# Kernel tuning notes

Measured on AMD Instinct MI355X. Metric: run time of the kernel, lower is better.

Reference implementation:

```python
import jax, jax.numpy as jnp
import numpy as np
from jax import lax

SD = 16  # sample_duration
POOL_KS = (SD, SD * 3 // 4, SD // 2, SD // 4)  # (16, 12, 8, 4)


def conv3d_same(x, w, b):
    # x: [B,C,T,H,W], w: [O,I,3,3,3]
    y = lax.conv_general_dilated(
        x, w, window_strides=(1, 1, 1), padding=[(1, 1), (1, 1), (1, 1)],
        dimension_numbers=("NCDHW", "OIDHW", "NCDHW"))
    return y + b[None, :, None, None, None]


def maxpool_t(x, k):
    # MaxPool3d((k,1,1), stride=1): max over sliding temporal window
    return lax.reduce_window(x, -jnp.inf, lax.max,
                             (1, 1, k, 1, 1), (1, 1, 1, 1, 1), "VALID")


def head1x1(x, w, b):
    # 1x1x1 Conv3d as einsum; x: [B,C,T,H,W], w: [O,C]
    return jnp.einsum("bcthw,oc->bothw", x, w) + b[None, :, None, None, None]


def cls_prob(score):
    # _RPN.reshape(x,2) -> softmax(dim=1) -> reshape back to [B,30,T,H,W]
    B, C, T, H, W = score.shape
    s2 = score.reshape(B, 2, (C * T) // 2, H, W)
    p = jax.nn.softmax(s2, axis=1)
    return p.reshape(B, C, T, H, W)


def setup_inputs() -> dict:
    key = jax.random.key(0)
    ks = jax.random.split(key, 12)
    din, B, H, W = 512, 2, 28, 28
    s = 0.05
    return {
        "base_feat": jax.random.normal(ks[0], (B, din, SD, H, W), jnp.float32),
        "im_info": jnp.ones((B, 3), jnp.float32) * 448.0,
        "gt_boxes": jax.random.uniform(ks[1], (B, 20, 5), jnp.float32),
        "gt_rois": jax.random.uniform(ks[2], (B, 20, SD, 5), jnp.float32),
        "W_conv": jax.random.normal(ks[3], (din, din, 3, 3, 3), jnp.float32) * 0.01,
        "b_conv": jnp.zeros((din,), jnp.float32),
        "W_cls": jax.random.normal(ks[4], (30, din), jnp.float32) * s,
        "b_cls": jnp.zeros((30,), jnp.float32),
        "W_bbox": jax.random.normal(ks[5], (960, din), jnp.float32) * s,
        "b_bbox": jnp.zeros((960,), jnp.float32),
        "W_bbox_34": jax.random.normal(ks[6], (720, din), jnp.float32) * s,
        "b_bbox_34": jnp.zeros((720,), jnp.float32),
        "W_bbox_2": jax.random.normal(ks[7], (480, din), jnp.float32) * s,
        "b_bbox_2": jnp.zeros((480,), jnp.float32),
        "W_bbox_4": jax.random.normal(ks[8], (240, din), jnp.float32) * s,
        "b_bbox_4": jnp.zeros((240,), jnp.float32),
    }


def reference(base_feat, im_info, gt_boxes, gt_rois,
              W_conv, b_conv, W_cls, b_cls,
              W_bbox, b_bbox, W_bbox_34, b_bbox_34,
              W_bbox_2, b_bbox_2, W_bbox_4, b_bbox_4):
    # RPN conv + relu
    x = jax.nn.relu(conv3d_same(base_feat, W_conv, b_conv))
    # four temporal max-pool branches (T' = 1, 5, 9, 13)
    pools = [maxpool_t(x, k) for k in POOL_KS]
    # NOTE: original code applies the SAME RPN_cls_score conv to all branches
    probs = tuple(cls_prob(head1x1(p, W_cls, b_cls)) for p in pools)
    bbox_ws = [(W_bbox, b_bbox), (W_bbox_34, b_bbox_34),
               (W_bbox_2, b_bbox_2), (W_bbox_4, b_bbox_4)]
    bboxes = tuple(head1x1(p, w, b) for p, (w, b) in zip(pools, bbox_ws))
    return probs + bboxes
```

## Files before the change

### kernel.cpp

```cpp
#include <hip/hip_runtime.h>

typedef unsigned short u16;
typedef unsigned int   u32;
typedef __bf16  bf16x8 __attribute__((ext_vector_type(8)));
typedef float   f32x4  __attribute__((ext_vector_type(4)));

__device__ __forceinline__ float bf2f(u16 u) {
    u32 v = ((u32)u) << 16;
    return __builtin_bit_cast(float, v);
}
__device__ __forceinline__ u16 f2bf(float f) {
    u32 u = __builtin_bit_cast(u32, f);
    return (u16)((u + 0x7FFFu + ((u >> 16) & 1u)) >> 16);
}
__device__ __forceinline__ float ldf(const void* p, long i, int f32) {
    return f32 ? ((const float*)p)[i] : bf2f(((const u16*)p)[i]);
}
__device__ __forceinline__ int is_f32(const u32* im) {
    return im[0] == 0x43E00000u;
}
__device__ __forceinline__ void gl2lds16(const u16* g, u16* l) {
    __builtin_amdgcn_global_load_lds(
        (const __attribute__((address_space(1))) void*)g,
        (__attribute__((address_space(3))) void*)l, 16, 0, 0);
}

__global__ void zero_kernel(uint4* __restrict__ p, const int n)
{
    int i = blockIdx.x * 256 + threadIdx.x;
    if (i < n) p[i] = uint4{0u, 0u, 0u, 0u};
}

__global__ void pad_fill(const void* __restrict__ src, u16* __restrict__ xpad,
                         const u32* __restrict__ im)
{
    const int f32 = is_f32(im);
    __shared__ u16 lds[56 * 40];
    int blk = blockIdx.x;
    const int h2  = blk % 14;  blk /= 14;
    const int c32 = blk & 15;  blk >>= 4;
    const int t   = blk & 15;
    const int b   = blk >> 4;
    const int tid = threadIdx.x;
    const long sbase = ((long)(b * 512 + c32 * 32) * 16 + t) * 784 + h2 * 56;
    #pragma unroll
    for (int it = tid; it < 1792; it += 256) {
        const int c = it / 56, p = it - c * 56;
        float v = f32 ? ((const float*)src)[sbase + (long)c * 12544 + p]
                      : bf2f(((const u16*)src)[sbase + (long)c * 12544 + p]);
        lds[p * 40 + c] = f2bf(v);
    }
    __syncthreads();
    if (tid < 224) {
        const int p = tid >> 2, g = tid & 3;
        const int h = h2 * 2 + p / 28, w = p % 28;
        const long o = (((long)(b * 18 + t + 1) * 30 + h + 1) * 30 + (w + 1)) * 512
                       + c32 * 32 + g * 8;
        *(uint4*)&xpad[o] = *(const uint4*)&lds[p * 40 + g * 8];
    }
}

__global__ void wt_transform(const void* __restrict__ wconv, u16* __restrict__ wt,
                             const u32* __restrict__ im)
{
    const int f32 = is_f32(im);
    __shared__ u16 lds[256 * 28];
    const int tid = threadIdx.x;
    const int pair_base = blockIdx.x * 256;
    const long s0 = (long)pair_base * 27;
    for (int it = tid; it < 256 * 27; it += 256) {
        const int p = it / 27, o = it - p * 27;
        float v = f32 ? ((const float*)wconv)[s0 + it]
                      : bf2f(((const u16*)wconv)[s0 + it]);
        lds[p * 28 + o] = f2bf(v);
    }
    __syncthreads();
    #pragma unroll
    for (int off = 0; off < 27; ++off)
        wt[(long)off * 262144 + pair_base + tid] = lds[tid * 28 + off];
}

__global__ void cvt_all(const void* s0, const void* s1, const void* s2,
                        const void* s3, const void* s4,
                        const void* b0, const void* b1, const void* b2,
                        const void* b3, const void* b4, const void* b5,
                        u16* __restrict__ whd, float* __restrict__ bfs,
                        const u32* __restrict__ im)
{
    const int f32 = is_f32(im);
    int i = blockIdx.x * 256 + threadIdx.x;
    if (i < 1244160) {
        const void* s; long j;
        if      (i < 15360)   { s = s0; j = i; }
        else if (i < 506880)  { s = s1; j = i - 15360; }
        else if (i < 875520)  { s = s2; j = i - 506880; }
        else if (i < 1121280) { s = s3; j = i - 875520; }
        else                  { s = s4; j = i - 1121280; }
        whd[i] = f2bf(ldf(s, j, f32));
        return;
    }
    i -= 1244160;
    if (i >= 2942) return;
    float v;
    if      (i < 512)  v = ldf(b0, i, f32);
    else if (i < 542)  v = ldf(b1, i - 512, f32);
    else if (i < 1502) v = ldf(b2, i - 542, f32);
    else if (i < 2222) v = ldf(b3, i - 1502, f32);
    else if (i < 2702) v = ldf(b4, i - 2222, f32);
    else               v = ldf(b5, i - 2702, f32);
    bfs[i] = v;
}

__global__ __launch_bounds__(512, 2) void conv_gemm256(
    const u16* __restrict__ xpad, const u16* __restrict__ wt,
    const float* __restrict__ bfs, u16* __restrict__ y)
{
    __shared__ u16 smem[65536];
    const int tid = threadIdx.x;

    const int bx  = blockIdx.x;
    const int xcd = bx & 7, pos = bx >> 3;
    const int L   = (xcd < 4 ? xcd * 25 : 100 + (xcd - 4) * 24) + pos;
    const int m_base = (L & 1) * 256;
    const int n_base = (L >> 1) * 256;

    const int rq  = tid >> 2;
    const int gsw = (((tid & 3) ^ ((tid >> 3) & 3))) * 8;
    const u16* pa0 = wt + (long)(m_base + rq) * 512 + gsw;
    const u16* pa1 = pa0 + 128 * 512;

    const int n0 = n_base + rq;
    const int n1 = n0 + 128;
    int b0 = n0 / 12544, r0 = n0 % 12544;
    int t0 = r0 / 784,   q0 = r0 % 784;
    int h0 = q0 / 28,    w0 = q0 % 28;
    int b1 = n1 / 12544, r1 = n1 % 12544;
    int t1 = r1 / 784,   q1 = r1 % 784;
    int h1 = q1 / 28,    w1 = q1 % 28;
    const int sa0 = ((b0 * 18 + t0) * 30 + h0) * 30 + w0;
    const int sa1 = ((b1 * 18 + t1) * 30 + h1) * 30 + w1;
    const u16* pb0 = xpad + (long)sa0 * 512 + gsw;
    const u16* pb1 = xpad + (long)sa1 * 512 + gsw;

    const int lane = tid & 63, wid = tid >> 6;
    const int l16 = lane & 15, quad = lane >> 4;
    const int wm = wid >> 2;
    const int wn = wid & 3;
    const int slot  = (quad ^ ((l16 >> 1) & 3)) * 8;
    const int aoffs = (wm * 128 + l16) * 32 + slot;
    const int boffs = 8192 + (wn * 64 + l16) * 32 + slot;

    f32x4 acc[8][4] = {};

    #pragma unroll
    for (int k = 0; k < 3; ++k) {
        u16* dst = smem + (k << 14);
        gl2lds16(pa0 + k * 32, dst + tid * 8);
        gl2lds16(pa1 + k * 32, dst + 4096  + tid * 8);
        gl2lds16(pb0 + k * 32, dst + 8192  + tid * 8);
        gl2lds16(pb1 + k * 32, dst + 12288 + tid * 8);
    }

#define KTILE(ktl, STG, GATE)                                                  \
    {                                                                          \
        asm volatile("s_waitcnt vmcnt(" #GATE ")" ::: "memory");               \
        asm volatile("s_barrier" ::: "memory");                                \
        const u16* buf = smem + (((ktl) & 3) << 14);                           \
        bf16x8 af[8], bfr[4];                                                  \
        _Pragma("unroll")                                                      \
        for (int mi = 0; mi < 4; ++mi)                                         \
            af[mi] = *(const bf16x8*)&buf[aoffs + mi * 512];                   \
        _Pragma("unroll")                                                      \
        for (int ni = 0; ni < 4; ++ni)                                         \
            bfr[ni] = *(const bf16x8*)&buf[boffs + ni * 512];                  \
        _Pragma("unroll")                                                      \
        for (int mi = 4; mi < 8; ++mi)                                         \
            af[mi] = *(const bf16x8*)&buf[aoffs + mi * 512];                   \
        if (STG) {                                                             \
            const int kts = (ktl) + 3;                                         \
            const int tap = kts >> 4, kc = kts & 15;                           \
            const int kd = tap / 9, r9 = tap - kd * 9;                         \
            const int kh = r9 / 3,  kw = r9 - kh * 3;                          \
            const long aoff = (long)tap * 262144 + kc * 32;                    \
            const long boff = (long)(kd * 900 + kh * 30 + kw) * 512 + kc * 32; \
            u16* dst = smem + ((kts & 3) << 14);                               \
            gl2lds16(pa0 + aoff, dst + tid * 8);                               \
            gl2lds16(pa1 + aoff, dst + 4096  + tid * 8);                       \
            gl2lds16(pb0 + boff, dst + 8192  + tid * 8);                       \
            gl2lds16(pb1 + boff, dst + 12288 + tid * 8);                       \
        }                                                                      \
        __builtin_amdgcn_s_setprio(1);                                         \
        _Pragma("unroll")                                                      \
        for (int mi = 0; mi < 4; ++mi)                                         \
            _Pragma("unroll")                                                  \
            for (int ni = 0; ni < 4; ++ni)                                     \
                acc[mi][ni] = __builtin_amdgcn_mfma_f32_16x16x32_bf16(         \
                    af[mi], bfr[ni], acc[mi][ni], 0, 0, 0);                    \
        _Pragma("unroll")                                                      \
        for (int mi = 4; mi < 8; ++mi)                                         \
            _Pragma("unroll")                                                  \
            for (int ni = 0; ni < 4; ++ni)                                     \
                acc[mi][ni] = __builtin_amdgcn_mfma_f32_16x16x32_bf16(         \
                    af[mi], bfr[ni], acc[mi][ni], 0, 0, 0);                    \
        __builtin_amdgcn_s_setprio(0);                                         \
    }

    for (int kt = 0; kt < 429; ++kt) KTILE(kt, 1, 8)
    KTILE(429, 0, 8)
    KTILE(430, 0, 4)
    KTILE(431, 0, 0)
#undef KTILE

    #pragma unroll
    for (int mi = 0; mi < 8; ++mi) {
        const int mrow = m_base + wm * 128 + mi * 16 + quad * 4;
        float bias[4];
        #pragma unroll
        for (int r = 0; r < 4; ++r) bias[r] = bfs[mrow + r];
        #pragma unroll
        for (int ni = 0; ni < 4; ++ni) {
            const int ng = n_base + wn * 64 + ni * 16 + l16;
            f32x4 a = acc[mi][ni];
            u16 o0 = f2bf(fmaxf(a[0] + bias[0], 0.f));
            u16 o1 = f2bf(fmaxf(a[1] + bias[1], 0.f));
            u16 o2 = f2bf(fmaxf(a[2] + bias[2], 0.f));
            u16 o3 = f2bf(fmaxf(a[3] + bias[3], 0.f));
            uint2 pv;
            pv.x = (u32)o0 | ((u32)o1 << 16);
            pv.y = (u32)o2 | ((u32)o3 << 16);
            *(uint2*)&y[(long)ng * 512 + mrow] = pv;
        }
    }
}

__device__ __forceinline__ uint4 max8(uint4 A, uint4 Bv)
{
    const u16* a = (const u16*)&A;
    const u16* b = (const u16*)&Bv;
    uint4 R;
    u16* r = (u16*)&R;
    #pragma unroll
    for (int i = 0; i < 8; ++i) r[i] = (bf2f(a[i]) >= bf2f(b[i])) ? a[i] : b[i];
    return R;
}

__global__ void pool_all(const u16* __restrict__ y, u16* __restrict__ p4,
                         u16* __restrict__ p8, u16* __restrict__ p12,
                         u16* __restrict__ p16)
{
    int g = blockIdx.x * 256 + threadIdx.x;
    if (g >= 100352) return;
    const int c8 = g & 63;
    int pos = g >> 6;
    const int hw = pos % 784; const int b = pos / 784;
    const u16* src = y + ((long)(b * 16) * 784 + hw) * 512 + c8 * 8;
    uint4 v[16];
    #pragma unroll
    for (int t = 0; t < 16; ++t)
        v[t] = *(const uint4*)(src + (long)t * 401408);
    uint4 pr[15];
    #pragma unroll
    for (int t = 0; t < 15; ++t) pr[t] = max8(v[t], v[t + 1]);
    uint4 qd[13];
    #pragma unroll
    for (int t = 0; t < 13; ++t) qd[t] = max8(pr[t], pr[t + 2]);
    uint4 e8[9];
    #pragma unroll
    for (int t = 0; t < 9; ++t) e8[t] = max8(qd[t], qd[t + 4]);
    uint4 e12[5];
    #pragma unroll
    for (int t = 0; t < 5; ++t) e12[t] = max8(e8[t], qd[t + 8]);
    uint4 e16 = max8(e8[0], e8[8]);

    const long col = (long)hw * 512 + c8 * 8;
    #pragma unroll
    for (int t = 0; t < 13; ++t)
        *(uint4*)&p4[((long)(b * 13 + t) * 784) * 512 + col] = qd[t];
    #pragma unroll
    for (int t = 0; t < 9; ++t)
        *(uint4*)&p8[((long)(b * 9 + t) * 784) * 512 + col] = e8[t];
    #pragma unroll
    for (int t = 0; t < 5; ++t)
        *(uint4*)&p12[((long)(b * 5 + t) * 784) * 512 + col] = e12[t];
    *(uint4*)&p16[((long)b * 784) * 512 + col] = e16;
}

__global__ __launch_bounds__(256, 2) void heads_gemm(
    const u16* __restrict__ p16, const u16* __restrict__ p12,
    const u16* __restrict__ p8,  const u16* __restrict__ p4,
    const u16* __restrict__ wcls, const u16* __restrict__ wb1,
    const u16* __restrict__ wb34, const u16* __restrict__ wb2,
    const u16* __restrict__ wb4,  const float* __restrict__ bfs,
    float* __restrict__ clsr, void* __restrict__ outv,
    const u32* __restrict__ im)
{
    const int f32 = is_f32(im);
    int bid = blockIdx.x;
    const u16* pool; const u16* wbp; int Ti, CH, nt, mt; long boff, coff, ooff;
    if (bid < 104)      {             nt = bid % 13;  mt = bid / 13;  pool = p16; wbp = wb1;  Ti = 1;  CH = 960; boff = 542;  coff = 0;      ooff = 1317120; }
    else if (bid < 476) { bid -= 104; nt = bid % 62;  mt = bid / 62;  pool = p12; wbp = wb34; Ti = 5;  CH = 720; boff = 1502; coff = 47040;  ooff = 2822400; }
    else if (bid < 920) { bid -= 476; nt = bid % 111; mt = bid / 111; pool = p8;  wbp = wb2;  Ti = 9;  CH = 480; boff = 2222; coff = 282240; ooff = 8467200; }
    else                { bid -= 920; nt = bid % 160; mt = bid / 160; pool = p4;  wbp = wb4;  Ti = 13; CH = 240; boff = 2702; coff = 705600; ooff = 15240960; }
    const int M = 30 + CH;
    const int THW = Ti * 784;
    const int N = 2 * THW;
    const int n_base = nt * 128;
    const int m_base = mt * 128;

    __shared__ u16 lds[32768];
    const int tid = threadIdx.x;
    const int lane = tid & 63;
    const int wid  = tid >> 6;
    const int quad = lane >> 4;
    const int l16  = lane & 15;
    const int wm = (wid & 1) * 64;
    const int wn = (wid >> 1) * 64;
    const int srow = tid >> 3;
    const int lc8  = ((tid & 7) ^ (srow & 7)) * 8;

    const u16* arow[4]; const u16* brow[4];
    #pragma unroll
    for (int j = 0; j < 4; ++j) {
        int m = m_base + j * 32 + srow; if (m > M - 1) m = M - 1;
        arow[j] = ((m < 30) ? (wcls + m * 512) : (wbp + (m - 30) * 512)) + lc8;
        int n = n_base + j * 32 + srow; if (n > N - 1) n = N - 1;
        brow[j] = pool + (long)n * 512 + lc8;
    }

    int rowA[4], rowB[4];
    #pragma unroll
    for (int i = 0; i < 4; ++i) {
        rowA[i] = (wm + i * 16 + l16) * 64;
        rowB[i] = 8192 + (wn + i * 16 + l16) * 64;
    }
    const int cx  = l16 & 7;
    const int ch0 = (quad ^ cx) * 8;
    const int ch1 = ((4 + quad) ^ cx) * 8;

    #pragma unroll
    for (int j = 0; j < 4; ++j)
        gl2lds16(arow[j], &lds[tid * 8 + j * 2048]);
    #pragma unroll
    for (int j = 0; j < 4; ++j)
        gl2lds16(brow[j], &lds[8192 + tid * 8 + j * 2048]);

    f32x4 acc[4][4] = {};
    for (int kc = 0; kc < 8; ++kc) {
        asm volatile("s_waitcnt vmcnt(0)" ::: "memory");
        asm volatile("s_barrier" ::: "memory");
        const u16* buf = lds + (kc & 1) * 16384;
        bf16x8 af[8], bfr[8];
        #pragma unroll
        for (int mi = 0; mi < 4; ++mi) {
            af[mi]     = *(const bf16x8*)&buf[rowA[mi] + ch0];
            af[mi + 4] = *(const bf16x8*)&buf[rowA[mi] + ch1];
        }
        #pragma unroll
        for (int ni = 0; ni < 4; ++ni) {
            bfr[ni]     = *(const bf16x8*)&buf[rowB[ni] + ch0];
            bfr[ni + 4] = *(const bf16x8*)&buf[rowB[ni] + ch1];
        }
        if (kc < 7) {
            u16* dst = lds + ((kc + 1) & 1) * 16384 + tid * 8;
            const int kcol = (kc + 1) * 64;
            #pragma unroll
            for (int j = 0; j < 4; ++j)
                gl2lds16(arow[j] + kcol, dst + j * 2048);
            #pragma unroll
            for (int j = 0; j < 4; ++j)
                gl2lds16(brow[j] + kcol, dst + 8192 + j * 2048);
        }
        __builtin_amdgcn_s_setprio(1);
        #pragma unroll
        for (int mi = 0; mi < 4; ++mi)
            #pragma unroll
            for (int ni = 0; ni < 4; ++ni)
                acc[mi][ni] = __builtin_amdgcn_mfma_f32_16x16x32_bf16(
                    af[mi], bfr[ni], acc[mi][ni], 0, 0, 0);
        #pragma unroll
        for (int mi = 0; mi < 4; ++mi)
            #pragma unroll
            for (int ni = 0; ni < 4; ++ni)
                acc[mi][ni] = __builtin_amdgcn_mfma_f32_16x16x32_bf16(
                    af[mi + 4], bfr[ni + 4], acc[mi][ni], 0, 0, 0);
        __builtin_amdgcn_s_setprio(0);
    }

    const float* bcls = bfs + 512;
    const float* bb   = bfs + boff;
    #pragma unroll
    for (int mi = 0; mi < 4; ++mi) {
        const int mrow = m_base + wm + mi * 16 + quad * 4;
        #pragma unroll
        for (int ni = 0; ni < 4; ++ni) {
            const int ng = n_base + wn + ni * 16 + l16;
            if (ng >= N) continue;
            const int b  = ng / THW;
            const int rr = ng % THW;
            f32x4 a = acc[mi][ni];
            #pragma unroll
            for (int r = 0; r < 4; ++r) {
                const int m = mrow + r;
                if (m >= M) break;
                const float bias = (m < 30) ? bcls[m] : bb[m - 30];
                const float v = a[r] + bias;
                if (m < 30) {
                    clsr[coff + ((long)(b * 30 + m)) * THW + rr] = v;
                } else {
                    const long oi = ooff + ((long)(b * CH + (m - 30))) * THW + rr;
                    if (f32) ((float*)outv)[oi] = v;
                    else     ((u16*)outv)[oi]   = f2bf(v);
                }
            }
        }
    }
}

__global__ void softmax_all(const float* __restrict__ clsr,
                            void* __restrict__ outv, const u32* __restrict__ im)
{
    const int f32 = is_f32(im);
    int g = blockIdx.x * 256 + threadIdx.x;
    if (g >= 658560) return;
    int Ti; long off;
    if      (g < 23520)  { Ti = 1;  off = 0; }
    else if (g < 141120) { Ti = 5;  off = 47040;  g -= 23520; }
    else if (g < 352800) { Ti = 9;  off = 282240; g -= 141120; }
    else                 { Ti = 13; off = 705600; g -= 352800; }
    const int THW = Ti * 784;
    const int rr = g % THW;
    int r2 = g / THW;
    const int j = r2 % 15; const int b = r2 / 15;
    const long i0 = off + ((long)(b * 30 + j)) * THW + rr;
    const long i1 = off + ((long)(b * 30 + j + 15)) * THW + rr;
    const float s0 = clsr[i0], s1 = clsr[i1];
    const float mx = fmaxf(s0, s1);
    const float e0 = __expf(s0 - mx), e1 = __expf(s1 - mx);
    const float inv = 1.0f / (e0 + e1);
    if (f32) {
        ((float*)outv)[i0] = e0 * inv;
        ((float*)outv)[i1] = e1 * inv;
    } else {
        ((u16*)outv)[i0] = f2bf(e0 * inv);
        ((u16*)outv)[i1] = f2bf(e1 * inv);
    }
}

extern "C" void kernel_launch(void* const* d_in, const int* in_sizes, int n_in,
                              void* d_out, int out_size, void* d_ws, size_t ws_size,
                              hipStream_t stream)
{
    const void* base_feat = d_in[0];
    const u32*  im_info   = (const u32*)d_in[1];
    const void* W_conv    = d_in[4];
    const void* b_conv    = d_in[5];
    const void* W_cls     = d_in[6];
    const void* b_cls     = d_in[7];
    const void* W_bbox    = d_in[8];
    const void* b_bbox    = d_in[9];
    const void* W_bbox34  = d_in[10];
    const void* b_bbox34  = d_in[11];
    const void* W_bbox2   = d_in[12];
    const void* b_bbox2   = d_in[13];
    const void* W_bbox4   = d_in[14];
    const void* b_bbox4   = d_in[15];

    char* ws = (char*)d_ws;
    u16*   xpad = (u16*)  (ws + 0);
    u16*   wt   = (u16*)  (ws + 33177600);
    u16*   y    = (u16*)  (ws + 47333376);
    u16*   p4   = (u16*)  (ws + 73023488);
    u16*   p8   = (u16*)  (ws + 93896704);
    u16*   p12  = (u16*)  (ws + 108347392);
    u16*   p16  = (u16*)  (ws + 116375552);
    float* clsr = (float*)(ws + 117981184);
    u16*   whd  = (u16*)  (ws + 123249728);
    float* bfs  = (float*)(ws + 125738048);

    u16* w_cls_b  = whd;
    u16* w_b1_b   = whd + 15360;
    u16* w_b34_b  = whd + 506880;
    u16* w_b2_b   = whd + 875520;
    u16* w_b4_b   = whd + 1121280;

    zero_kernel<<<8100, 256, 0, stream>>>((uint4*)xpad, 2073600);
    pad_fill<<<7168, 256, 0, stream>>>(base_feat, xpad, im_info);
    wt_transform<<<1024, 256, 0, stream>>>(W_conv, wt, im_info);
    cvt_all<<<4873, 256, 0, stream>>>(W_cls, W_bbox, W_bbox34, W_bbox2, W_bbox4,
                                      b_conv, b_cls, b_bbox, b_bbox34, b_bbox2,
                                      b_bbox4, whd, bfs, im_info);

    conv_gemm256<<<196, 512, 0, stream>>>(xpad, wt, bfs, y);

    pool_all<<<392, 256, 0, stream>>>(y, p4, p8, p12, p16);

    heads_gemm<<<1400, 256, 0, stream>>>(p16, p12, p8, p4,
                                         w_cls_b, w_b1_b, w_b34_b, w_b2_b, w_b4_b,
                                         bfs, clsr, d_out, im_info);

    softmax_all<<<2573, 256, 0, stream>>>(clsr, d_out, im_info);
}
```

Measured before the change: 622.5 us.

## Narrow pool_all to 4-channel threads and single-buffer heads_gemm LDS

pool_all now has each thread handle 4 channels with 8-byte loads and stores, doubling the grid to get more threads in flight. heads_gemm drops its double-buffered LDS prefetch pipeline in favour of single-buffered A/B tiles with __syncthreads around each K step, which halves LDS use. The single buffer no longer overlaps global loads with MFMA work, so load latency is exposed at every K step. It also removes the setprio hints.

New measurement: 571.6 us. 1.09x faster.

```diff
diff --git a/kernel.cpp b/kernel.cpp
--- a/kernel.cpp
+++ b/kernel.cpp
@@ -233,14 +233,14 @@
     }
 }
 
-__device__ __forceinline__ uint4 max8(uint4 A, uint4 Bv)
+__device__ __forceinline__ uint2 max4(uint2 A, uint2 Bv)
 {
     const u16* a = (const u16*)&A;
     const u16* b = (const u16*)&Bv;
-    uint4 R;
+    uint2 R;
     u16* r = (u16*)&R;
     #pragma unroll
-    for (int i = 0; i < 8; ++i) r[i] = (bf2f(a[i]) >= bf2f(b[i])) ? a[i] : b[i];
+    for (int i = 0; i < 4; ++i) r[i] = (bf2f(a[i]) >= bf2f(b[i])) ? a[i] : b[i];
     return R;
 }
 
@@ -249,40 +249,40 @@
                          u16* __restrict__ p16)
 {
     int g = blockIdx.x * 256 + threadIdx.x;
-    if (g >= 100352) return;
-    const int c8 = g & 63;
-    int pos = g >> 6;
+    if (g >= 200704) return;
+    const int c4 = g & 127;
+    int pos = g >> 7;
     const int hw = pos % 784; const int b = pos / 784;
-    const u16* src = y + ((long)(b * 16) * 784 + hw) * 512 + c8 * 8;
-    uint4 v[16];
+    const u16* src = y + ((long)(b * 16) * 784 + hw) * 512 + c4 * 4;
+    uint2 v[16];
     #pragma unroll
     for (int t = 0; t < 16; ++t)
-        v[t] = *(const uint4*)(src + (long)t * 401408);
-    uint4 pr[15];
-    #pragma unroll
-    for (int t = 0; t < 15; ++t) pr[t] = max8(v[t], v[t + 1]);
-    uint4 qd[13];
-    #pragma unroll
-    for (int t = 0; t < 13; ++t) qd[t] = max8(pr[t], pr[t + 2]);
-    uint4 e8[9];
-    #pragma unroll
-    for (int t = 0; t < 9; ++t) e8[t] = max8(qd[t], qd[t + 4]);
-    uint4 e12[5];
-    #pragma unroll
-    for (int t = 0; t < 5; ++t) e12[t] = max8(e8[t], qd[t + 8]);
-    uint4 e16 = max8(e8[0], e8[8]);
-
-    const long col = (long)hw * 512 + c8 * 8;
+        v[t] = *(const uint2*)(src + (long)t * 401408);
+    uint2 pr[15];
+    #pragma unroll
+    for (int t = 0; t < 15; ++t) pr[t] = max4(v[t], v[t + 1]);
+    uint2 qd[13];
+    #pragma unroll
+    for (int t = 0; t < 13; ++t) qd[t] = max4(pr[t], pr[t + 2]);
+    uint2 e8[9];
+    #pragma unroll
+    for (int t = 0; t < 9; ++t) e8[t] = max4(qd[t], qd[t + 4]);
+    uint2 e12[5];
+    #pragma unroll
+    for (int t = 0; t < 5; ++t) e12[t] = max4(e8[t], qd[t + 8]);
+    uint2 e16 = max4(e8[0], e8[8]);
+
+    const long col = (long)hw * 512 + c4 * 4;
     #pragma unroll
     for (int t = 0; t < 13; ++t)
-        *(uint4*)&p4[((long)(b * 13 + t) * 784) * 512 + col] = qd[t];
+        *(uint2*)&p4[((long)(b * 13 + t) * 784) * 512 + col] = qd[t];
     #pragma unroll
     for (int t = 0; t < 9; ++t)
-        *(uint4*)&p8[((long)(b * 9 + t) * 784) * 512 + col] = e8[t];
+        *(uint2*)&p8[((long)(b * 9 + t) * 784) * 512 + col] = e8[t];
     #pragma unroll
     for (int t = 0; t < 5; ++t)
-        *(uint4*)&p12[((long)(b * 5 + t) * 784) * 512 + col] = e12[t];
-    *(uint4*)&p16[((long)b * 784) * 512 + col] = e16;
+        *(uint2*)&p12[((long)(b * 5 + t) * 784) * 512 + col] = e12[t];
+    *(uint2*)&p16[((long)b * 784) * 512 + col] = e16;
 }
 
 __global__ __launch_bounds__(256, 2) void heads_gemm(
@@ -307,7 +307,8 @@
     const int n_base = nt * 128;
     const int m_base = mt * 128;
 
-    __shared__ u16 lds[32768];
+    __shared__ u16 lds_a[128 * 64];
+    __shared__ u16 lds_b[128 * 64];
     const int tid = threadIdx.x;
     const int lane = tid & 63;
     const int wid  = tid >> 6;
@@ -327,65 +328,48 @@
         brow[j] = pool + (long)n * 512 + lc8;
     }
 
+    u16* ldst_a = &lds_a[tid * 8];
+    u16* ldst_b = &lds_b[tid * 8];
+
     int rowA[4], rowB[4];
     #pragma unroll
     for (int i = 0; i < 4; ++i) {
         rowA[i] = (wm + i * 16 + l16) * 64;
-        rowB[i] = 8192 + (wn + i * 16 + l16) * 64;
+        rowB[i] = (wn + i * 16 + l16) * 64;
     }
     const int cx  = l16 & 7;
     const int ch0 = (quad ^ cx) * 8;
     const int ch1 = ((4 + quad) ^ cx) * 8;
 
-    #pragma unroll
-    for (int j = 0; j < 4; ++j)
-        gl2lds16(arow[j], &lds[tid * 8 + j * 2048]);
-    #pragma unroll
-    for (int j = 0; j < 4; ++j)
-        gl2lds16(brow[j], &lds[8192 + tid * 8 + j * 2048]);
-
     f32x4 acc[4][4] = {};
     for (int kc = 0; kc < 8; ++kc) {
-        asm volatile("s_waitcnt vmcnt(0)" ::: "memory");
-        asm volatile("s_barrier" ::: "memory");
-        const u16* buf = lds + (kc & 1) * 16384;
-        bf16x8 af[8], bfr[8];
-        #pragma unroll
-        for (int mi = 0; mi < 4; ++mi) {
-            af[mi]     = *(const bf16x8*)&buf[rowA[mi] + ch0];
-            af[mi + 4] = *(const bf16x8*)&buf[rowA[mi] + ch1];
-        }
-        #pragma unroll
-        for (int ni = 0; ni < 4; ++ni) {
-            bfr[ni]     = *(const bf16x8*)&buf[rowB[ni] + ch0];
-            bfr[ni + 4] = *(const bf16x8*)&buf[rowB[ni] + ch1];
-        }
-        if (kc < 7) {
-            u16* dst = lds + ((kc + 1) & 1) * 16384 + tid * 8;
-            const int kcol = (kc + 1) * 64;
+        const int kcol = kc * 64;
+        #pragma unroll
+        for (int j = 0; j < 4; ++j)
+            gl2lds16(arow[j] + kcol, ldst_a + j * 2048);
+        #pragma unroll
+        for (int j = 0; j < 4; ++j)
+            gl2lds16(brow[j] + kcol, ldst_b + j * 2048);
+        __syncthreads();
+        #pragma unroll
+        for (int h = 0; h < 2; ++h) {
+            const int co = h ? ch1 : ch0;
+            bf16x8 af[4], bfr[4];
             #pragma unroll
-            for (int j = 0; j < 4; ++j)
-                gl2lds16(arow[j] + kcol, dst + j * 2048);
-            #pragma unroll
-            for (int j = 0; j < 4; ++j)
-                gl2lds16(brow[j] + kcol, dst + 8192 + j * 2048);
-        }
-        __builtin_amdgcn_s_setprio(1);
-        #pragma unroll
-        for (int mi = 0; mi < 4; ++mi)
+            for (int mi = 0; mi < 4; ++mi)
+                af[mi]  = *(const bf16x8*)&lds_a[rowA[mi] + co];
             #pragma unroll
             for (int ni = 0; ni < 4; ++ni)
-                acc[mi][ni] = __builtin_amdgcn_mfma_f32_16x16x32_bf16(
-                    af[mi], bfr[ni], acc[mi][ni], 0, 0, 0);
-        #pragma unroll
-        for (int mi = 0; mi < 4; ++mi)
+                bfr[ni] = *(const bf16x8*)&lds_b[rowB[ni] + co];
             #pragma unroll
-            for (int ni = 0; ni < 4; ++ni)
-                acc[mi][ni] = __builtin_amdgcn_mfma_f32_16x16x32_bf16(
-                    af[mi + 4], bfr[ni + 4], acc[mi][ni], 0, 0, 0);
-        __builtin_amdgcn_s_setprio(0);
-    }
-
+            for (int mi = 0; mi < 4; ++mi)
+                #pragma unroll
+                for (int ni = 0; ni < 4; ++ni)
+                    acc[mi][ni] = __builtin_amdgcn_mfma_f32_16x16x32_bf16(
+                        af[mi], bfr[ni], acc[mi][ni], 0, 0, 0);
+        }
+        __syncthreads();
+    }
     const float* bcls = bfs + 512;
     const float* bb   = bfs + boff;
     #pragma unroll
@@ -492,7 +476,7 @@
 
     conv_gemm256<<<196, 512, 0, stream>>>(xpad, wt, bfs, y);
 
-    pool_all<<<392, 256, 0, stream>>>(y, p4, p8, p12, p16);
+    pool_all<<<784, 256, 0, stream>>>(y, p4, p8, p12, p16);
 
     heads_gemm<<<1400, 256, 0, stream>>>(p16, p12, p8, p4,
                                          w_cls_b, w_b1_b, w_b34_b, w_b2_b, w_b4_b,
```
